# Optimization experiments

Measured on AMD Instinct MI355X. Metric: run time of the kernel, lower is better.

The kernel has to match this reference:

```python
import jax, jax.numpy as jnp
import numpy as np

B, F, V, E = 4096, 26, 20000, 64
LAYERS = [256, 128, 1]


def setup_inputs() -> dict:
    key = jax.random.key(0)
    ks = jax.random.split(key, 13)
    s = 1.0 / np.sqrt(E)
    inp = {
        "x_idx": jax.random.randint(ks[0], (B, F), 0, V),
        # per-field embedding tables [F, V, E] and linear (bias) tables [F, V, 1]
        "embed_w": jax.random.normal(ks[1], (F, V, E), jnp.float32) * 0.01,
        "embed_b": jax.random.normal(ks[2], (F, V, 1), jnp.float32) * 0.01,
        "attention_w": jax.random.normal(ks[3], (E, E), jnp.float32) * s,
        "attention_b": jax.random.normal(ks[4], (1, E), jnp.float32) * 0.01,
        "attention_p": jax.random.normal(ks[5], (E,), jnp.float32) * 0.01,
        "w0": jax.random.normal(ks[6], (E, LAYERS[0]), jnp.float32) * s,
        "b0": jnp.zeros((LAYERS[0],), jnp.float32),
        "w1": jax.random.normal(ks[7], (LAYERS[0], LAYERS[1]), jnp.float32) * (1.0 / np.sqrt(LAYERS[0])),
        "b1": jnp.zeros((LAYERS[1],), jnp.float32),
        "w2": jax.random.normal(ks[8], (LAYERS[1], LAYERS[2]), jnp.float32) * (1.0 / np.sqrt(LAYERS[1])),
        "b2": jnp.zeros((LAYERS[2],), jnp.float32),
        "bias": jnp.zeros((1,), jnp.float32),
    }
    return inp


def _gather_fields(tables, idx):
    # tables: [F, V, D], idx: [B, F] -> [B, F, D]
    return jax.vmap(lambda tbl, i: tbl[i], in_axes=(0, 1), out_axes=1)(tables, idx)


def reference(x_idx, embed_w, embed_b, attention_w, attention_b, attention_p,
              w0, b0, w1, b1, w2, b2, bias):
    f = embed_w.shape[0]
    xw = _gather_fields(embed_w, x_idx)                      # [B, F, E]
    iu, ju = jnp.triu_indices(f, k=1)                        # P = F*(F-1)/2 pairs, loop order i<j
    pairs = xw[:, iu, :] * xw[:, ju, :]                      # [B, P, E] pairwise FM interactions
    # attention network: relu(pairs @ W + b), score = <p, .>, softmax over pairs
    att_h = jax.nn.relu(jnp.einsum('bpe,ef->bpf', pairs, attention_w) + attention_b)
    scores = jnp.sum(attention_p * att_h, axis=2, keepdims=True)   # [B, P, 1]
    att_out = jax.nn.softmax(scores, axis=1)                       # softmax pooling over pairs
    afm = jnp.sum(att_out * pairs, axis=1)                         # [B, E]
    # MLP head
    h = jax.nn.relu(afm @ w0 + b0)
    h = jax.nn.relu(h @ w1 + b1)
    bilinear = h @ w2 + b2                                         # [B, 1]
    # linear (LR) term from per-field bias tables
    lr = jnp.sum(_gather_fields(embed_b, x_idx), axis=1)           # [B, 1]
    return bilinear + lr + bias
```

## Files before the change

kernel.cpp:

```cpp
#include <hip/hip_runtime.h>
#include <stdint.h>

#define B_N 4096
#define F_N 26
#define V_N 20000
#define E_N 64
#define P_N 325
#define PT  21

typedef __attribute__((ext_vector_type(8))) _Float16 half8;
typedef __attribute__((ext_vector_type(4))) _Float16 half4;
typedef __attribute__((ext_vector_type(4))) float floatx4;

__global__ __launch_bounds__(256, 4) void anfm_attn_kernel(
    const int* __restrict__ x_idx, const float* __restrict__ embed_w,
    const float* __restrict__ embed_b, const float* __restrict__ att_w,
    const float* __restrict__ att_b, const float* __restrict__ att_p,
    float* __restrict__ ws_afm, float* __restrict__ ws_lr)
{
    __shared__ _Float16 xwb[4][F_N][72];
    __shared__ _Float16 WT[64][72];
    __shared__ unsigned short pijL[336];
    __shared__ int   sIdx[4][F_N];
    __shared__ float lrbuf[4][F_N];
    __shared__ float apL[64], abL[64];

    const int tid  = threadIdx.x;
    const int lane = tid & 63;
    const int wid  = tid >> 6;
    const int c16  = lane & 15;
    const int g    = lane >> 4;
    const int b    = blockIdx.x * 4 + wid;

    if (tid < 4 * F_N) {
        int s = tid / F_N, f = tid - s * F_N;
        int idx = x_idx[(blockIdx.x * 4 + s) * F_N + f];
        sIdx[s][f]  = idx;
        lrbuf[s][f] = embed_b[f * V_N + idx];
    }
    for (int p = tid; p < 336; p += 256) {
        int i = 0, j = 1;
        if (p < P_N) {
            i = (int)((51.0f - sqrtf(2601.0f - 8.0f * (float)p)) * 0.5f);
            if (i * (51 - i) / 2 > p) i--;
            else if ((i + 1) * (50 - i) / 2 <= p) i++;
            j = p - i * (51 - i) / 2 + i + 1;
        }
        pijL[p] = (unsigned short)((i << 8) | j);
    }
    if (tid < 64)                   apL[tid]      = att_p[tid];
    else if (tid < 128)             abL[tid - 64] = att_b[tid - 64];
    for (int idx = tid; idx < 64 * 64; idx += 256) {
        int k = idx >> 6, col = idx & 63;
        WT[col][k] = (_Float16)att_w[idx];
    }
    __syncthreads();

    half8 bfr[4][2];
    #pragma unroll
    for (int nt = 0; nt < 4; nt++)
        #pragma unroll
        for (int s = 0; s < 2; s++)
            bfr[nt][s] = *reinterpret_cast<const half8*>(
                &WT[nt * 16 + c16][s * 32 + g * 8]);

    #pragma unroll
    for (int it = 0; it < 7; it++) {
        int f = it * 4 + g;
        if (f < F_N) {
            const float4* src = reinterpret_cast<const float4*>(
                embed_w + ((size_t)(f * V_N + sIdx[wid][f])) * E_N);
            float4 v = src[c16];
            half4 hv = {(_Float16)v.x, (_Float16)v.y, (_Float16)v.z, (_Float16)v.w};
            *reinterpret_cast<half4*>(&xwb[wid][f][c16 * 4]) = hv;
        }
    }

    float acf[16];
    #pragma unroll
    for (int u = 0; u < 16; u++) acf[u] = 0.f;
    float Zp = 0.f;

    #pragma unroll 1
    for (int t = 0; t < PT; t++) {
        int pk = pijL[t * 16 + c16];
        int ri = pk >> 8, rj = pk & 255;
        half8 af[2];
        #pragma unroll
        for (int s = 0; s < 2; s++) {
            half8 xv = *reinterpret_cast<const half8*>(&xwb[wid][ri][s * 32 + g * 8]);
            half8 yv = *reinterpret_cast<const half8*>(&xwb[wid][rj][s * 32 + g * 8]);
            af[s] = xv * yv;
        }
        float scq = 0.f;
        #pragma unroll
        for (int nt = 0; nt < 4; nt++) {
            floatx4 acc = *reinterpret_cast<const floatx4*>(&abL[nt * 16 + g * 4]);
            acc = __builtin_amdgcn_mfma_f32_16x16x32_f16(bfr[nt][0], af[0], acc, 0, 0, 0);
            acc = __builtin_amdgcn_mfma_f32_16x16x32_f16(bfr[nt][1], af[1], acc, 0, 0, 0);
            floatx4 ap4 = *reinterpret_cast<const floatx4*>(&apL[nt * 16 + g * 4]);
            #pragma unroll
            for (int r = 0; r < 4; r++)
                scq = fmaf(ap4[r], fmaxf(acc[r], 0.f), scq);
        }
        scq += __shfl_xor(scq, 16);
        scq += __shfl_xor(scq, 32);
        float w = (t * 16 + c16 < P_N) ? __expf(scq) : 0.f;
        Zp += w;
        #pragma unroll
        for (int s = 0; s < 2; s++)
            #pragma unroll
            for (int u = 0; u < 8; u++)
                acf[s * 8 + u] = fmaf((float)af[s][u], w, acf[s * 8 + u]);
    }

    #pragma unroll
    for (int msk = 1; msk <= 8; msk <<= 1) {
        Zp += __shfl_xor(Zp, msk);
        #pragma unroll
        for (int u = 0; u < 16; u++) acf[u] += __shfl_xor(acf[u], msk);
    }

    if (c16 == 0) {
        float rZ = 1.f / Zp;
        #pragma unroll
        for (int s = 0; s < 2; s++) {
            floatx4 o0 = {acf[s * 8 + 0] * rZ, acf[s * 8 + 1] * rZ,
                          acf[s * 8 + 2] * rZ, acf[s * 8 + 3] * rZ};
            floatx4 o1 = {acf[s * 8 + 4] * rZ, acf[s * 8 + 5] * rZ,
                          acf[s * 8 + 6] * rZ, acf[s * 8 + 7] * rZ};
            *reinterpret_cast<floatx4*>(&ws_afm[(size_t)b * 64 + s * 32 + g * 8])     = o0;
            *reinterpret_cast<floatx4*>(&ws_afm[(size_t)b * 64 + s * 32 + g * 8 + 4]) = o1;
        }
    }
    float lv = (lane < F_N) ? lrbuf[wid][lane] : 0.f;
    #pragma unroll
    for (int off = 32; off; off >>= 1) lv += __shfl_xor(lv, off);
    if (lane == 0) ws_lr[b] = lv;
}

__global__ __launch_bounds__(256, 4) void anfm_mlp_kernel(
    const float* __restrict__ ws_afm, const float* __restrict__ ws_lr,
    const float* __restrict__ w0, const float* __restrict__ b0,
    const float* __restrict__ w1, const float* __restrict__ b1,
    const float* __restrict__ w2, const float* __restrict__ b2,
    const float* __restrict__ bias, float* __restrict__ out)
{
    __shared__ _Float16 afmL[16][72];
    __shared__ _Float16 h0L[16][264];
    __shared__ float    h1L[16][132];

    const int tid  = threadIdx.x;
    const int lane = tid & 63;
    const int wid  = tid >> 6;
    const int c16  = lane & 15;
    const int g    = lane >> 4;
    const int blk  = blockIdx.x;

    for (int it = tid; it < 16 * 64; it += 256) {
        int s = it >> 6, e = it & 63;
        afmL[s][e] = (_Float16)ws_afm[((size_t)blk * 16 + s) * 64 + e];
    }
    __syncthreads();

    {
        half8 af[2];
        #pragma unroll
        for (int s = 0; s < 2; s++)
            af[s] = *reinterpret_cast<const half8*>(&afmL[c16][s * 32 + g * 8]);
        #pragma unroll
        for (int q = 0; q < 4; q++) {
            int n = (wid * 4 + q) * 16 + c16;
            half8 bf[2];
            #pragma unroll
            for (int s = 0; s < 2; s++)
                #pragma unroll
                for (int u = 0; u < 8; u++)
                    bf[s][u] = (_Float16)w0[(s * 32 + g * 8 + u) * 256 + n];
            floatx4 acc = {0.f, 0.f, 0.f, 0.f};
            acc = __builtin_amdgcn_mfma_f32_16x16x32_f16(af[0], bf[0], acc, 0, 0, 0);
            acc = __builtin_amdgcn_mfma_f32_16x16x32_f16(af[1], bf[1], acc, 0, 0, 0);
            float b0n = b0[n];
            #pragma unroll
            for (int r = 0; r < 4; r++)
                h0L[g * 4 + r][n] = (_Float16)fmaxf(acc[r] + b0n, 0.f);
        }
    }
    __syncthreads();

    #pragma unroll
    for (int q = 0; q < 2; q++) {
        int n = (wid * 2 + q) * 16 + c16;
        floatx4 acc = {0.f, 0.f, 0.f, 0.f};
        #pragma unroll
        for (int ks = 0; ks < 8; ks++) {
            half8 af = *reinterpret_cast<const half8*>(&h0L[c16][ks * 32 + g * 8]);
            half8 bf;
            #pragma unroll
            for (int u = 0; u < 8; u++)
                bf[u] = (_Float16)w1[(ks * 32 + g * 8 + u) * 128 + n];
            acc = __builtin_amdgcn_mfma_f32_16x16x32_f16(af, bf, acc, 0, 0, 0);
        }
        float b1n = b1[n];
        #pragma unroll
        for (int r = 0; r < 4; r++)
            h1L[g * 4 + r][n] = fmaxf(acc[r] + b1n, 0.f);
    }
    __syncthreads();

    float w2a = w2[lane * 2], w2b = w2[lane * 2 + 1];
    float base = b2[0] + bias[0];
    #pragma unroll
    for (int s = 0; s < 4; s++) {
        int m = wid * 4 + s;
        float part = fmaf(h1L[m][lane * 2], w2a, h1L[m][lane * 2 + 1] * w2b);
        #pragma unroll
        for (int off = 32; off; off >>= 1) part += __shfl_xor(part, off);
        if (lane == 0) {
            int sg = blk * 16 + m;
            out[sg] = part + base + ws_lr[sg];
        }
    }
}

extern "C" void kernel_launch(void* const* d_in, const int* in_sizes, int n_in,
                              void* d_out, int out_size, void* d_ws, size_t ws_size,
                              hipStream_t stream) {
    const int*   x_idx   = (const int*)d_in[0];
    const float* embed_w = (const float*)d_in[1];
    const float* embed_b = (const float*)d_in[2];
    const float* att_w   = (const float*)d_in[3];
    const float* att_b   = (const float*)d_in[4];
    const float* att_p   = (const float*)d_in[5];
    const float* w0      = (const float*)d_in[6];
    const float* b0      = (const float*)d_in[7];
    const float* w1      = (const float*)d_in[8];
    const float* b1      = (const float*)d_in[9];
    const float* w2      = (const float*)d_in[10];
    const float* b2      = (const float*)d_in[11];
    const float* bias    = (const float*)d_in[12];

    float* ws_afm = (float*)d_ws;
    float* ws_lr  = ws_afm + (size_t)B_N * E_N;
    float* out    = (float*)d_out;

    anfm_attn_kernel<<<B_N / 4, 256, 0, stream>>>(x_idx, embed_w, embed_b,
                                                  att_w, att_b, att_p,
                                                  ws_afm, ws_lr);
    anfm_mlp_kernel<<<B_N / 16, 256, 0, stream>>>(ws_afm, ws_lr,
                                                  w0, b0, w1, b1, w2, b2, bias, out);
}
```

Baseline: 41.80 us.

## Issue embedding gathers before setup barrier and use 8 samples per block

```diff
diff --git a/kernel.cpp b/kernel.cpp
--- a/kernel.cpp
+++ b/kernel.cpp
@@ -7,22 +7,21 @@
 #define E_N 64
 #define P_N 325
 #define PT  21
+#define SPB 8
 
 typedef __attribute__((ext_vector_type(8))) _Float16 half8;
 typedef __attribute__((ext_vector_type(4))) _Float16 half4;
 typedef __attribute__((ext_vector_type(4))) float floatx4;
 
-__global__ __launch_bounds__(256, 4) void anfm_attn_kernel(
+__global__ __launch_bounds__(512, 2) void anfm_attn_kernel(
     const int* __restrict__ x_idx, const float* __restrict__ embed_w,
     const float* __restrict__ embed_b, const float* __restrict__ att_w,
     const float* __restrict__ att_b, const float* __restrict__ att_p,
     float* __restrict__ ws_afm, float* __restrict__ ws_lr)
 {
-    __shared__ _Float16 xwb[4][F_N][72];
+    __shared__ _Float16 xwb[SPB][F_N][72];
     __shared__ _Float16 WT[64][72];
     __shared__ unsigned short pijL[336];
-    __shared__ int   sIdx[4][F_N];
-    __shared__ float lrbuf[4][F_N];
     __shared__ float apL[64], abL[64];
 
     const int tid  = threadIdx.x;
@@ -30,15 +29,23 @@
     const int wid  = tid >> 6;
     const int c16  = lane & 15;
     const int g    = lane >> 4;
-    const int b    = blockIdx.x * 4 + wid;
-
-    if (tid < 4 * F_N) {
-        int s = tid / F_N, f = tid - s * F_N;
-        int idx = x_idx[(blockIdx.x * 4 + s) * F_N + f];
-        sIdx[s][f]  = idx;
-        lrbuf[s][f] = embed_b[f * V_N + idx];
-    }
-    for (int p = tid; p < 336; p += 256) {
+    const int b    = blockIdx.x * SPB + wid;
+
+    int myidx = (lane < F_N) ? x_idx[b * F_N + lane] : 0;
+    float lv  = (lane < F_N) ? embed_b[lane * V_N + myidx] : 0.f;
+    float4 gv[7];
+    #pragma unroll
+    for (int it = 0; it < 7; it++) {
+        int f = it * 4 + g;
+        int fc = (f < F_N) ? f : 0;
+        int idxf = __shfl(myidx, fc);
+        const float4* src = reinterpret_cast<const float4*>(
+            embed_w + ((size_t)(fc * V_N + idxf)) * E_N);
+        gv[it] = src[c16];
+    }
+
+    if (tid < 336) {
+        int p = tid;
         int i = 0, j = 1;
         if (p < P_N) {
             i = (int)((51.0f - sqrtf(2601.0f - 8.0f * (float)p)) * 0.5f);
@@ -47,12 +54,24 @@
             j = p - i * (51 - i) / 2 + i + 1;
         }
         pijL[p] = (unsigned short)((i << 8) | j);
-    }
-    if (tid < 64)                   apL[tid]      = att_p[tid];
-    else if (tid < 128)             abL[tid - 64] = att_b[tid - 64];
-    for (int idx = tid; idx < 64 * 64; idx += 256) {
+    } else if (tid < 400) {
+        apL[tid - 336] = att_p[tid - 336];
+    } else if (tid < 464) {
+        abL[tid - 400] = att_b[tid - 400];
+    }
+    for (int idx = tid; idx < 64 * 64; idx += 512) {
         int k = idx >> 6, col = idx & 63;
         WT[col][k] = (_Float16)att_w[idx];
+    }
+
+    #pragma unroll
+    for (int it = 0; it < 7; it++) {
+        int f = it * 4 + g;
+        if (f < F_N) {
+            float4 v = gv[it];
+            half4 hv = {(_Float16)v.x, (_Float16)v.y, (_Float16)v.z, (_Float16)v.w};
+            *reinterpret_cast<half4*>(&xwb[wid][f][c16 * 4]) = hv;
+        }
     }
     __syncthreads();
 
@@ -63,18 +82,6 @@
         for (int s = 0; s < 2; s++)
             bfr[nt][s] = *reinterpret_cast<const half8*>(
                 &WT[nt * 16 + c16][s * 32 + g * 8]);
-
-    #pragma unroll
-    for (int it = 0; it < 7; it++) {
-        int f = it * 4 + g;
-        if (f < F_N) {
-            const float4* src = reinterpret_cast<const float4*>(
-                embed_w + ((size_t)(f * V_N + sIdx[wid][f])) * E_N);
-            float4 v = src[c16];
-            half4 hv = {(_Float16)v.x, (_Float16)v.y, (_Float16)v.z, (_Float16)v.w};
-            *reinterpret_cast<half4*>(&xwb[wid][f][c16 * 4]) = hv;
-        }
-    }
 
     float acf[16];
     #pragma unroll
@@ -133,7 +140,6 @@
             *reinterpret_cast<floatx4*>(&ws_afm[(size_t)b * 64 + s * 32 + g * 8 + 4]) = o1;
         }
     }
-    float lv = (lane < F_N) ? lrbuf[wid][lane] : 0.f;
     #pragma unroll
     for (int off = 32; off; off >>= 1) lv += __shfl_xor(lv, off);
     if (lane == 0) ws_lr[b] = lv;
@@ -244,9 +250,9 @@
     float* ws_lr  = ws_afm + (size_t)B_N * E_N;
     float* out    = (float*)d_out;
 
-    anfm_attn_kernel<<<B_N / 4, 256, 0, stream>>>(x_idx, embed_w, embed_b,
-                                                  att_w, att_b, att_p,
-                                                  ws_afm, ws_lr);
+    anfm_attn_kernel<<<B_N / SPB, 512, 0, stream>>>(x_idx, embed_w, embed_b,
+                                                    att_w, att_b, att_p,
+                                                    ws_afm, ws_lr);
     anfm_mlp_kernel<<<B_N / 16, 256, 0, stream>>>(ws_afm, ws_lr,
                                                   w0, b0, w1, b1, w2, b2, bias, out);
 }
```

New measurement: 42.20 us. No clear change (+1.0%).
